# Performance work log

Hardware: AMD Instinct MI355X
Metric: run time of the kernel (lower is better)

## Reference

```python
import jax, jax.numpy as jnp
import numpy as np

B, SL = 16, 512
S = SL - 1            # context length after shift (length=1)
E = 256               # embedding_size / hidden_size
NH = 4                # num_heads
K = 4                 # conv1d_kernel_size
I = 2 * E             # mLSTM inner dim (_inner_embedding_dim = 2*E)
DHM = I // NH         # mLSTM head dim
DHS = E // NH         # sLSTM head dim
NB, BS = I // 4, 4    # qkv_proj_blocksize=4 block-diagonal projections
F = 384               # gated FFN up dim = round_up(1.3*256, 64)
NUM_SKILLS, NUM_Q = 500, 10000
EPS = 1e-5


def _ln(x, w):
    mu = x.mean(-1, keepdims=True)
    var = x.var(-1, keepdims=True)
    return (x - mu) / jnp.sqrt(var + EPS) * w


def _causal_dwconv(x, w, b):
    # x: (B,S,C), depthwise causal conv with kernel (C,K)
    xt = jnp.transpose(x, (0, 2, 1))
    y = jax.lax.conv_general_dilated(
        xt, w[:, None, :], (1,), [(K - 1, 0)],
        dimension_numbers=('NCH', 'OIH', 'NCH'),
        feature_group_count=x.shape[-1])
    return jnp.transpose(y, (0, 2, 1)) + b


def _headwise(x, w):
    # block-diagonal linear: w (NB, BS, BS)
    xb = x.reshape(x.shape[0], x.shape[1], NB, BS)
    return jnp.einsum('bsnd,nod->bsno', xb, w).reshape(x.shape)


def _forward(questions, responses, skills,
             q_embed, qa_embed, q_embed_diff, qa_embed_diff, difficult_param,
             ln0_w, m_up_w, m_up_b, m_conv_w, m_conv_b, m_q_w, m_k_w, m_v_w,
             m_ig_w, m_ig_b, m_fg_w, m_fg_b, m_outnorm_w, m_skip, m_down_w, m_down_b,
             ln1_w, s_conv_w, s_conv_b, s_gate_w, s_rec_w, s_bias, s_gn_w,
             ln2_w, ffn_up_w, ffn_up_b, ffn_down_w, ffn_down_b,
             postnorm_w, out_w1, out_b1, out_w2, out_b2, out_w3, out_b3):
    pid = questions[:, :-1]
    q_data = skills[:, :-1]
    q_shft = skills[:, 1:]
    target = (responses * (responses > -1).astype(responses.dtype))[:, :-1]

    q_e = q_embed[q_data]                              # (B,S,E)
    qa_e = qa_embed[target] + q_e
    pid_e = difficult_param[pid]                       # (B,S,1)
    q_e = q_e + pid_e * q_embed_diff[q_data]
    qa_e = qa_e + pid_e * qa_embed_diff[target]

    # ---- xLSTM stack: block 0 = mLSTM block, block 1 = sLSTM block + gated FFN ----
    x = qa_e  # dropout is identity in eval

    # mLSTM block: x = x + mlstm_layer(LN(x))
    h = _ln(x, ln0_w)
    up = h @ m_up_w.T + m_up_b                         # (B,S,2I)
    x_m, z = jnp.split(up, 2, axis=-1)
    xc = jax.nn.silu(_causal_dwconv(x_m, m_conv_w, m_conv_b))
    q = _headwise(xc, m_q_w)
    k = _headwise(xc, m_k_w)
    v = _headwise(x_m, m_v_w)
    ifin = jnp.concatenate([q, k, v], axis=-1)         # (B,S,3I)
    ig = jnp.einsum('bsf,hf->bhs', ifin, m_ig_w) + m_ig_b[None, :, None]
    fg = jnp.einsum('bsf,hf->bhs', ifin, m_fg_w) + m_fg_b[None, :, None]
    qh = q.reshape(B, S, NH, DHM).transpose(0, 2, 1, 3)
    kh = k.reshape(B, S, NH, DHM).transpose(0, 2, 1, 3)
    vh = v.reshape(B, S, NH, DHM).transpose(0, 2, 1, 3)
    # parallel stabilized mLSTM
    logf = jax.nn.log_sigmoid(fg)                      # (B,NH,S)
    cs = jnp.concatenate([jnp.zeros((B, NH, 1), logf.dtype), jnp.cumsum(logf, -1)], -1)
    dmat = cs[:, :, 1:, None] - cs[:, :, None, 1:]     # (B,NH,S,S): sum of logf over (s,t]
    ltr = jnp.tril(jnp.ones((S, S), bool))
    logD = jnp.where(ltr, dmat, -jnp.inf) + ig[:, :, None, :]
    maxD = jnp.max(logD, -1, keepdims=True)
    D = jnp.exp(logD - maxD)
    qk = jnp.einsum('bhtd,bhsd->bhts', qh, kh) * (DHM ** -0.5)
    C = qk * D
    norm = jnp.maximum(jnp.abs(C.sum(-1, keepdims=True)), jnp.exp(-maxD))
    hh = jnp.einsum('bhts,bhsd->bhtd', C / (norm + 1e-6), vh)
    # multi-head layernorm (per head over DHM), weight on flattened dim
    hn = (hh - hh.mean(-1, keepdims=True)) / jnp.sqrt(hh.var(-1, keepdims=True) + EPS)
    hflat = hn.transpose(0, 2, 1, 3).reshape(B, S, I) * m_outnorm_w
    hout = (hflat + m_skip * xc) * jax.nn.silu(z)
    x = x + (hout @ m_down_w.T + m_down_b)

    # sLSTM block: x = x + slstm_layer(LN(x)); x = x + ffn(LN(x))
    h = _ln(x, ln1_w)
    hc = jax.nn.silu(_causal_dwconv(h, s_conv_w, s_conv_b))
    hh4 = h.reshape(B, S, NH, DHS)
    hc4 = hc.reshape(B, S, NH, DHS)
    gi = jnp.einsum('bsnd,nod->bsno', hc4, s_gate_w[0])   # i,f from conv path
    gf = jnp.einsum('bsnd,nod->bsno', hc4, s_gate_w[1])
    gz = jnp.einsum('bsnd,nod->bsno', hh4, s_gate_w[2])   # z,o from x path
    go = jnp.einsum('bsnd,nod->bsno', hh4, s_gate_w[3])
    wx = jnp.stack([gi, gf, gz, go], axis=2) + s_bias[None, None]  # (B,S,4,NH,DHS)

    def step(carry, wx_t):
        y, c, n, m = carry
        raw = wx_t + jnp.einsum('bnd,gnde->bgne', y, s_rec_w)
        iraw, fraw, zraw, oraw = raw[:, 0], raw[:, 1], raw[:, 2], raw[:, 3]
        logfplusm = m + jax.nn.log_sigmoid(fraw)
        mnew = jnp.maximum(iraw, logfplusm)
        ig_ = jnp.exp(iraw - mnew)
        fg_ = jnp.exp(logfplusm - mnew)
        cnew = fg_ * c + ig_ * jnp.tanh(zraw)
        nnew = fg_ * n + ig_
        ynew = jax.nn.sigmoid(oraw) * cnew / nnew
        return (ynew, cnew, nnew, mnew), ynew

    z0 = jnp.zeros((B, NH, DHS), x.dtype)
    _, ys = jax.lax.scan(step, (z0, z0, z0, z0), jnp.swapaxes(wx, 0, 1))
    y = jnp.swapaxes(ys, 0, 1)                           # (B,S,NH,DHS)
    yn = (y - y.mean(-1, keepdims=True)) / jnp.sqrt(y.var(-1, keepdims=True) + EPS)
    x = x + yn.reshape(B, S, E) * s_gn_w

    # gated FFN (relu)
    h = _ln(x, ln2_w)
    gate, upf = jnp.split(h @ ffn_up_w.T + ffn_up_b, 2, axis=-1)
    x = x + (jax.nn.relu(gate) * upf) @ ffn_down_w.T + ffn_down_b

    d = _ln(x, postnorm_w)                               # post_blocks_norm

    fam = jnp.where((target == 1)[..., None], d, 0.0)
    unfam = jnp.where((target == 0)[..., None], d, 0.0)
    d2 = d - pid_e
    cq = jnp.concatenate([d2, q_e, fam, unfam], axis=-1)  # (B,S,4E)
    o = jax.nn.relu(cq @ out_w1.T + out_b1)
    o = jax.nn.relu(o @ out_w2.T + out_b2)
    probs = jax.nn.sigmoid(o @ out_w3.T + out_b3)
    pred = jnp.take_along_axis(probs, q_shft[..., None], axis=-1)[..., 0]
    return pred                                          # (B,S)


def setup_inputs():
    key = jax.random.key(0)
    ks = iter(jax.random.split(key, 64))
    def rn(shape, s=0.02):
        return jax.random.normal(next(ks), shape, jnp.float32) * s
    return dict(
        questions=jax.random.randint(next(ks), (B, SL), 0, NUM_Q),
        responses=jax.random.randint(next(ks), (B, SL), 0, 2),
        skills=jax.random.randint(next(ks), (B, SL), 0, NUM_SKILLS),
        attention_mask=jnp.ones((B, SL), jnp.int32),
        q_embed=rn((NUM_SKILLS, E), 1.0),
        qa_embed=rn((2, E), 1.0),
        q_embed_diff=rn((NUM_SKILLS + 1, E), 1.0),
        qa_embed_diff=rn((2 * NUM_SKILLS + 1, E), 1.0),
        difficult_param=rn((NUM_Q + 1, 1), 0.1),
        ln0_w=jnp.ones((E,)),
        m_up_w=rn((2 * I, E)), m_up_b=jnp.zeros((2 * I,)),
        m_conv_w=rn((I, K), 0.1), m_conv_b=jnp.zeros((I,)),
        m_q_w=rn((NB, BS, BS), 0.1), m_k_w=rn((NB, BS, BS), 0.1), m_v_w=rn((NB, BS, BS), 0.1),
        m_ig_w=rn((NH, 3 * I)), m_ig_b=jnp.zeros((NH,)),
        m_fg_w=rn((NH, 3 * I)), m_fg_b=jnp.zeros((NH,)),
        m_outnorm_w=jnp.ones((I,)), m_skip=jnp.ones((I,)),
        m_down_w=rn((E, I)), m_down_b=jnp.zeros((E,)),
        ln1_w=jnp.ones((E,)),
        s_conv_w=rn((E, K), 0.1), s_conv_b=jnp.zeros((E,)),
        s_gate_w=rn((4, NH, DHS, DHS), 0.1),
        s_rec_w=rn((4, NH, DHS, DHS), 0.05),
        s_bias=jnp.zeros((4, NH, DHS)),
        s_gn_w=jnp.ones((E,)),
        ln2_w=jnp.ones((E,)),
        ffn_up_w=rn((2 * F, E)), ffn_up_b=jnp.zeros((2 * F,)),
        ffn_down_w=rn((E, F)), ffn_down_b=jnp.zeros((E,)),
        postnorm_w=jnp.ones((E,)),
        out_w1=rn((2 * E, 4 * E)), out_b1=jnp.zeros((2 * E,)),
        out_w2=rn((E, 2 * E)), out_b2=jnp.zeros((E,)),
        out_w3=rn((NUM_SKILLS, E)), out_b3=jnp.zeros((NUM_SKILLS,)),
    )


def reference(questions, responses, skills, attention_mask,
              q_embed, qa_embed, q_embed_diff, qa_embed_diff, difficult_param,
              ln0_w, m_up_w, m_up_b, m_conv_w, m_conv_b, m_q_w, m_k_w, m_v_w,
              m_ig_w, m_ig_b, m_fg_w, m_fg_b, m_outnorm_w, m_skip, m_down_w, m_down_b,
              ln1_w, s_conv_w, s_conv_b, s_gate_w, s_rec_w, s_bias, s_gn_w,
              ln2_w, ffn_up_w, ffn_up_b, ffn_down_w, ffn_down_b,
              postnorm_w, out_w1, out_b1, out_w2, out_b2, out_w3, out_b3):
    return _forward(questions, responses, skills,
                    q_embed, qa_embed, q_embed_diff, qa_embed_diff, difficult_param,
                    ln0_w, m_up_w, m_up_b, m_conv_w, m_conv_b, m_q_w, m_k_w, m_v_w,
                    m_ig_w, m_ig_b, m_fg_w, m_fg_b, m_outnorm_w, m_skip, m_down_w, m_down_b,
                    ln1_w, s_conv_w, s_conv_b, s_gate_w, s_rec_w, s_bias, s_gn_w,
                    ln2_w, ffn_up_w, ffn_up_b, ffn_down_w, ffn_down_b,
                    postnorm_w, out_w1, out_b1, out_w2, out_b2, out_w3, out_b3)
```

## Files before the change

kernel.cpp:

```cpp
#include <hip/hip_runtime.h>
#include <hip/hip_bf16.h>

#define B_    16
#define SL_   512
#define S_    511
#define E_    256
#define NH_   4
#define I_    512
#define DHM_  128
#define DHS_  64
#define F_    384
#define NP_   8192
#define NROW  (B_*S_)
#define EPS_  1e-5f

typedef __hip_bfloat16 bf16;
typedef unsigned short u16;
typedef __bf16 bf16x8v __attribute__((ext_vector_type(8)));
typedef float  f32x4v  __attribute__((ext_vector_type(4)));

__device__ __forceinline__ float rcp_(float x){ return __builtin_amdgcn_rcpf(x); }
__device__ __forceinline__ float sig_(float x){ return rcp_(1.f+__expf(-x)); }
__device__ __forceinline__ float silu_(float x){ return x*sig_(x); }
__device__ __forceinline__ float logsig_(float x){ return fminf(x,0.f) - __logf(1.f + __expf(-fabsf(x))); }
__device__ __forceinline__ float expneg_(float x){ return __expf(fminf(x,0.f)); }
__device__ __forceinline__ float expclamp_(float x){ return __expf(fminf(fmaxf(x,-80.f),80.f)); }
__device__ __forceinline__ float tanh_(float x){ return 1.f - 2.f*rcp_(__expf(2.f*x)+1.f); }

__global__ __launch_bounds__(256) void k_prep(
  const float* __restrict__ m_down_w, bf16* __restrict__ m_down_w16,
  const float* __restrict__ ffn_up_w, bf16* __restrict__ ffn_up_w16,
  const float* __restrict__ ffn_down_w, bf16* __restrict__ ffn_down_w16,
  const float* __restrict__ out_w1, bf16* __restrict__ out_w1_16,
  const float* __restrict__ out_w2, bf16* __restrict__ out_w2_16,
  const float* __restrict__ m_up_w, bf16* __restrict__ m_up_whi, bf16* __restrict__ m_up_wlo,
  const float* __restrict__ s_gate_w, float* __restrict__ gwT,
  const float* __restrict__ s_rec_w, bf16* __restrict__ wfrag)
{
  int i = blockIdx.x*256 + threadIdx.x;
  if (i < 131072){ m_down_w16[i] = __float2bfloat16(m_down_w[i]); return; }
  i -= 131072;
  if (i < 196608){
    int rp=i>>8, c=i&255; int j=rp>>1, p=rp&1;
    ffn_up_w16[i] = __float2bfloat16(ffn_up_w[(size_t)(j + p*F_)*E_ + c]); return;
  }
  i -= 196608;
  if (i < 98304){ ffn_down_w16[i] = __float2bfloat16(ffn_down_w[i]); return; }
  i -= 98304;
  if (i < 524288){ out_w1_16[i] = __float2bfloat16(out_w1[i]); return; }
  i -= 524288;
  if (i < 131072){ out_w2_16[i] = __float2bfloat16(out_w2[i]); return; }
  i -= 131072;
  if (i < 262144){
    float v = m_up_w[i];
    bf16 h = __float2bfloat16(v);
    m_up_whi[i]=h;
    m_up_wlo[i]=__float2bfloat16(v-__bfloat162float(h));
    return;
  }
  i -= 262144;
  if (i < 65536){
    int blk=i>>12, d=(i>>6)&63, e=i&63;
    gwT[(size_t)(blk*64+d)*64+e] = s_gate_w[(size_t)(blk*64+e)*64+d]; return;
  }
  i -= 65536;
  {
    int j=i&7, l=(i>>3)&63, kf=(i>>9)&1, t=(i>>10)&15, n=i>>14;
    int g=t>>2;
    int e=(t&3)*16 + (l&15);
    int d=(l>>4)*16 + kf*8 + j;
    wfrag[i] = __float2bfloat16(s_rec_w[((size_t)((g*4+n)*64 + d))*64 + e]);
  }
}

__global__ __launch_bounds__(256) void k_embed(
  const int* __restrict__ questions, const int* __restrict__ responses, const int* __restrict__ skills,
  const float* __restrict__ q_embed, const float* __restrict__ qa_embed,
  const float* __restrict__ q_embed_diff, const float* __restrict__ qa_embed_diff,
  const float* __restrict__ difficult_param, const float* __restrict__ ln0w,
  float* __restrict__ x, float* __restrict__ qe,
  bf16* __restrict__ h_hi, bf16* __restrict__ h_lo,
  float* __restrict__ pide, int* __restrict__ tgt, int* __restrict__ qsh)
{
  __shared__ float red[256];
  int r = blockIdx.x; int e = threadIdx.x;
  float xa = 0.f;
  if (r < NROW){
    int b = r / S_, s = r % S_;
    int pid  = questions[b*SL_+s];
    int qd   = skills[b*SL_+s];
    int resp = responses[b*SL_+s];
    int t    = (resp > -1) ? resp : 0;
    float pe = difficult_param[pid];
    float q0 = q_embed[qd*E_+e];
    xa = q0 + qa_embed[t*E_+e] + pe*qa_embed_diff[t*E_+e];
    float qn = q0 + pe*q_embed_diff[qd*E_+e];
    x[(size_t)r*E_+e]=xa; qe[(size_t)r*E_+e]=qn;
    if (e==0){ pide[r]=pe; tgt[r]=t; qsh[r]=skills[b*SL_+s+1]; }
  } else {
    x[(size_t)r*E_+e]=0.f; qe[(size_t)r*E_+e]=0.f;
    if (e==0){ pide[r]=0.f; tgt[r]=-7; qsh[r]=0; }
  }
  red[e]=xa; __syncthreads();
  for(int s2=128;s2>0;s2>>=1){ if(e<s2) red[e]+=red[e+s2]; __syncthreads(); }
  float mu = red[0]*(1.f/E_); __syncthreads();
  float d = xa-mu;
  red[e]=d*d; __syncthreads();
  for(int s2=128;s2>0;s2>>=1){ if(e<s2) red[e]+=red[e+s2]; __syncthreads(); }
  float var = red[0]*(1.f/E_);
  float o = d*rsqrtf(var+EPS_)*ln0w[e];
  bf16 hv = __float2bfloat16(o);
  h_hi[(size_t)r*E_+e] = hv;
  h_lo[(size_t)r*E_+e] = __float2bfloat16(o-__bfloat162float(hv));
}

__global__ __launch_bounds__(256) void k_ln(
  const float* __restrict__ in, const float* __restrict__ w, float* __restrict__ out)
{
  __shared__ float red[256];
  int r = blockIdx.x, t = threadIdx.x;
  float v = in[(size_t)r*E_+t];
  red[t]=v; __syncthreads();
  for(int s=128;s>0;s>>=1){ if(t<s) red[t]+=red[t+s]; __syncthreads(); }
  float mu = red[0]*(1.f/E_); __syncthreads();
  float d = v-mu;
  red[t]=d*d; __syncthreads();
  for(int s=128;s>0;s>>=1){ if(t<s) red[t]+=red[t+s]; __syncthreads(); }
  float var = red[0]*(1.f/E_);
  out[(size_t)r*E_+t] = d*rsqrtf(var+EPS_)*w[t];
}

__global__ __launch_bounds__(256) void k_gemm16s(
  const bf16* __restrict__ Ah, const bf16* __restrict__ Al,
  const bf16* __restrict__ Bh, const bf16* __restrict__ Bl,
  const float* __restrict__ bias, float* __restrict__ C, int M, int K)
{
  int tid=threadIdx.x;
  int wave=tid>>6, lane=tid&63;
  int wr=wave>>1, wc=wave&1;
  int row0=blockIdx.y*64 + wr*32;
  int col0=blockIdx.x*64 + wc*32;
  int lrow = lane&15, lq = lane>>4;
  f32x4v acc[2][2] = {};
  size_t aoff = (size_t)(row0+lrow)*K + lq*8;
  size_t boff = (size_t)(col0+lrow)*K + lq*8;
  for(int k0=0;k0<K;k0+=32){
    bf16x8v ah0=*(const bf16x8v*)(Ah+aoff+k0), ah1=*(const bf16x8v*)(Ah+aoff+(size_t)16*K+k0);
    bf16x8v al0=*(const bf16x8v*)(Al+aoff+k0), al1=*(const bf16x8v*)(Al+aoff+(size_t)16*K+k0);
    bf16x8v bh0=*(const bf16x8v*)(Bh+boff+k0), bh1=*(const bf16x8v*)(Bh+boff+(size_t)16*K+k0);
    bf16x8v bl0=*(const bf16x8v*)(Bl+boff+k0), bl1=*(const bf16x8v*)(Bl+boff+(size_t)16*K+k0);
    acc[0][0]=__builtin_amdgcn_mfma_f32_16x16x32_bf16(ah0,bh0,acc[0][0],0,0,0);
    acc[0][1]=__builtin_amdgcn_mfma_f32_16x16x32_bf16(ah0,bh1,acc[0][1],0,0,0);
    acc[1][0]=__builtin_amdgcn_mfma_f32_16x16x32_bf16(ah1,bh0,acc[1][0],0,0,0);
    acc[1][1]=__builtin_amdgcn_mfma_f32_16x16x32_bf16(ah1,bh1,acc[1][1],0,0,0);
    acc[0][0]=__builtin_amdgcn_mfma_f32_16x16x32_bf16(ah0,bl0,acc[0][0],0,0,0);
    acc[0][1]=__builtin_amdgcn_mfma_f32_16x16x32_bf16(ah0,bl1,acc[0][1],0,0,0);
    acc[1][0]=__builtin_amdgcn_mfma_f32_16x16x32_bf16(ah1,bl0,acc[1][0],0,0,0);
    acc[1][1]=__builtin_amdgcn_mfma_f32_16x16x32_bf16(ah1,bl1,acc[1][1],0,0,0);
    acc[0][0]=__builtin_amdgcn_mfma_f32_16x16x32_bf16(al0,bh0,acc[0][0],0,0,0);
    acc[0][1]=__builtin_amdgcn_mfma_f32_16x16x32_bf16(al0,bh1,acc[0][1],0,0,0);
    acc[1][0]=__builtin_amdgcn_mfma_f32_16x16x32_bf16(al1,bh0,acc[1][0],0,0,0);
    acc[1][1]=__builtin_amdgcn_mfma_f32_16x16x32_bf16(al1,bh1,acc[1][1],0,0,0);
  }
  #pragma unroll
  for(int mi=0;mi<2;mi++){
    #pragma unroll
    for(int ni=0;ni<2;ni++){
      #pragma unroll
      for(int r=0;r<4;r++){
        int row=row0+mi*16+lq*4+r;
        int col=col0+ni*16+lrow;
        C[(size_t)row*M+col]=acc[mi][ni][r] + bias[col];
      }
    }
  }
}

__global__ __launch_bounds__(256) void k_gemm16(
  const bf16* __restrict__ A, const bf16* __restrict__ Bw,
  const float* __restrict__ bias, const float* __restrict__ resid,
  float* __restrict__ C, bf16* __restrict__ C16,
  int M, int K, int relu)
{
  int tid=threadIdx.x;
  int wave=tid>>6, lane=tid&63;
  int wr=wave>>1, wc=wave&1;
  int row0=blockIdx.y*64 + wr*32;
  int col0=blockIdx.x*64 + wc*32;
  int lrow = lane&15, lq = lane>>4;
  f32x4v acc[2][2] = {};
  const bf16* Abase = A  + (size_t)(row0+lrow)*K + lq*8;
  const bf16* Bbase = Bw + (size_t)(col0+lrow)*K + lq*8;
  for(int k0=0;k0<K;k0+=32){
    bf16x8v a0 = *(const bf16x8v*)(Abase + k0);
    bf16x8v a1 = *(const bf16x8v*)(Abase + (size_t)16*K + k0);
    bf16x8v b0 = *(const bf16x8v*)(Bbase + k0);
    bf16x8v b1 = *(const bf16x8v*)(Bbase + (size_t)16*K + k0);
    acc[0][0]=__builtin_amdgcn_mfma_f32_16x16x32_bf16(a0,b0,acc[0][0],0,0,0);
    acc[0][1]=__builtin_amdgcn_mfma_f32_16x16x32_bf16(a0,b1,acc[0][1],0,0,0);
    acc[1][0]=__builtin_amdgcn_mfma_f32_16x16x32_bf16(a1,b0,acc[1][0],0,0,0);
    acc[1][1]=__builtin_amdgcn_mfma_f32_16x16x32_bf16(a1,b1,acc[1][1],0,0,0);
  }
  #pragma unroll
  for(int mi=0;mi<2;mi++){
    #pragma unroll
    for(int ni=0;ni<2;ni++){
      #pragma unroll
      for(int r=0;r<4;r++){
        int row=row0+mi*16+lq*4+r;
        int col=col0+ni*16+lrow;
        float v=acc[mi][ni][r] + (bias? bias[col]:0.f);
        if(relu) v=fmaxf(v,0.f);
        if(resid) v += resid[(size_t)row*M+col];
        if(C)   C[(size_t)row*M+col]=v;
        if(C16) C16[(size_t)row*M+col]=__float2bfloat16(v);
      }
    }
  }
}

__global__ __launch_bounds__(256) void k_gemm16f(
  const bf16* __restrict__ A, const bf16* __restrict__ Bw,
  const float* __restrict__ bias, bf16* __restrict__ out, int K)
{
  int tid=threadIdx.x;
  int wave=tid>>6, lane=tid&63;
  int wr=wave>>1, wc=wave&1;
  int row0=blockIdx.y*64 + wr*32;
  int col0=blockIdx.x*64 + wc*32;
  int lrow = lane&15, lq = lane>>4;
  f32x4v acc[2][2] = {};
  const bf16* Abase = A  + (size_t)(row0+lrow)*K + lq*8;
  const bf16* Bbase = Bw + (size_t)(col0+lrow)*K + lq*8;
  for(int k0=0;k0<K;k0+=32){
    bf16x8v a0 = *(const bf16x8v*)(Abase + k0);
    bf16x8v a1 = *(const bf16x8v*)(Abase + (size_t)16*K + k0);
    bf16x8v b0 = *(const bf16x8v*)(Bbase + k0);
    bf16x8v b1 = *(const bf16x8v*)(Bbase + (size_t)16*K + k0);
    acc[0][0]=__builtin_amdgcn_mfma_f32_16x16x32_bf16(a0,b0,acc[0][0],0,0,0);
    acc[0][1]=__builtin_amdgcn_mfma_f32_16x16x32_bf16(a0,b1,acc[0][1],0,0,0);
    acc[1][0]=__builtin_amdgcn_mfma_f32_16x16x32_bf16(a1,b0,acc[1][0],0,0,0);
    acc[1][1]=__builtin_amdgcn_mfma_f32_16x16x32_bf16(a1,b1,acc[1][1],0,0,0);
  }
  #pragma unroll
  for(int mi=0;mi<2;mi++){
    #pragma unroll
    for(int ni=0;ni<2;ni++){
      #pragma unroll
      for(int r=0;r<4;r++){
        int row=row0+mi*16+lq*4+r;
        int col=col0+ni*16+lrow;
        float v=acc[mi][ni][r] + bias[(col>>1) + (col&1)*F_];
        float o = __shfl_xor(v, 1, 64);
        if(!(lrow&1)){
          out[(size_t)row*F_ + (col>>1)] = __float2bfloat16(fmaxf(v,0.f)*o);
        }
      }
    }
  }
}

__global__ __launch_bounds__(256) void k_conv_silu(
  const float* __restrict__ in, int ild, const float* __restrict__ w, const float* __restrict__ bws,
  float* __restrict__ out, int old_, int C)
{
  int i = blockIdx.x*256 + threadIdx.x;
  int r = i / C, c = i % C;
  if (r >= NP_) return;
  float acc = 0.f;
  if (r < NROW) {
    int b=r/S_, s=r%S_;
    acc = bws[c];
    #pragma unroll
    for(int j=0;j<4;j++){
      int ss=s-3+j;
      if(ss>=0) acc += w[c*4+j] * in[(size_t)(b*S_+ss)*ild + c];
    }
    acc = silu_(acc);
  }
  out[(size_t)r*old_ + c] = acc;
}

__global__ __launch_bounds__(256) void k_mega(
  const float* __restrict__ A,
  const float* __restrict__ cw, const float* __restrict__ cb,
  const float* __restrict__ wq, const float* __restrict__ wk, const float* __restrict__ wv,
  const float* __restrict__ wig, const float* __restrict__ big,
  const float* __restrict__ wfg, const float* __restrict__ bfg,
  float* __restrict__ xcout,
  bf16* __restrict__ qhi, bf16* __restrict__ qlo,
  bf16* __restrict__ khi, bf16* __restrict__ klo,
  bf16* __restrict__ vhi, bf16* __restrict__ vlo,
  float* __restrict__ igb, float* __restrict__ fgb)
{
  __shared__ float xcs[512];
  __shared__ float xms[512];
  __shared__ float qs[512], ks[512], vs[512];
  int r = blockIdx.x;
  int tid = threadIdx.x;
  if (r >= NROW){
    bf16 z = __float2bfloat16(0.f);
    size_t o = (size_t)r*512 + tid*2;
    qhi[o]=z; qhi[o+1]=z; qlo[o]=z; qlo[o+1]=z;
    khi[o]=z; khi[o+1]=z; klo[o]=z; klo[o+1]=z;
    vhi[o]=z; vhi[o+1]=z; vlo[o]=z; vlo[o+1]=z;
    return;
  }
  int b=r/S_, s=r%S_;
  const float* arow = A + (size_t)r*1024;
  for (int c=tid; c<512; c+=256){
    float acc = cb[c];
    #pragma unroll
    for(int j=0;j<4;j++){
      int ss=s-3+j;
      if(ss>=0) acc += cw[c*4+j]*A[((size_t)(b*S_+ss))*1024 + c];
    }
    acc = silu_(acc);
    xcs[c]=acc;
    xcout[(size_t)r*512+c]=acc;
    xms[c]=arow[c];
  }
  __syncthreads();
  for (int c=tid; c<512; c+=256){
    int n=c>>2, o=c&3;
    float aq=0.f, ak=0.f, av=0.f;
    #pragma unroll
    for(int d=0;d<4;d++){
      aq += xcs[n*4+d]*wq[(n*4+o)*4+d];
      ak += xcs[n*4+d]*wk[(n*4+o)*4+d];
      av += xms[n*4+d]*wv[(n*4+o)*4+d];
    }
    qs[c]=aq; ks[c]=ak; vs[c]=av;
    size_t oi=(size_t)r*512+c;
    bf16 qh=__float2bfloat16(aq); qhi[oi]=qh; qlo[oi]=__float2bfloat16(aq-__bfloat162float(qh));
    bf16 kh=__float2bfloat16(ak); khi[oi]=kh; klo[oi]=__float2bfloat16(ak-__bfloat162float(kh));
    bf16 vh=__float2bfloat16(av); vhi[oi]=vh; vlo[oi]=__float2bfloat16(av-__bfloat162float(vh));
  }
  __syncthreads();
  int h = tid>>6, lane = tid&63;
  float ai=0.f, af=0.f;
  for(int f=lane; f<1536; f+=64){
    float val = (f<512)? qs[f] : (f<1024)? ks[f-512] : vs[f-1024];
    ai += val*wig[h*1536+f];
    af += val*wfg[h*1536+f];
  }
  for(int m=32;m;m>>=1){ ai+=__shfl_xor(ai,m,64); af+=__shfl_xor(af,m,64); }
  if(lane==0){
    igb[(b*4+h)*512+s]=ai+big[h];
    fgb[(b*4+h)*512+s]=af+bfg[h];
  }
}

__global__ __launch_bounds__(256) void k_decay(
  const float* __restrict__ igb, const float* __restrict__ fgb,
  float* __restrict__ cs1, float* __restrict__ g, float* __restrict__ M)
{
  int bh = blockIdx.x; int tid = threadIdx.x;
  __shared__ float buf[512];
  __shared__ float buf2[512];
  for (int s=tid; s<512; s+=256)
    buf[s] = (s<S_) ? logsig_(fgb[bh*512+s]) : 0.f;
  __syncthreads();
  for (int off=1; off<512; off<<=1){
    int s0=tid, s1=tid+256;
    float v0 = buf[s0] + ((s0>=off)? buf[s0-off] : 0.f);
    float v1 = buf[s1] + ((s1>=off)? buf[s1-off] : 0.f);
    __syncthreads();
    buf[s0]=v0; buf[s1]=v1;
    __syncthreads();
  }
  for (int s=tid; s<512; s+=256){
    float c = buf[s];
    if (s<S_){
      cs1[bh*512+s]=c;
      float gv = igb[bh*512+s]-c;
      g[bh*512+s]=gv;
      buf2[s]=gv;
    } else buf2[s] = -3.4e38f;
  }
  __syncthreads();
  for (int off=1; off<512; off<<=1){
    int s0=tid, s1=tid+256;
    float v0 = fmaxf(buf2[s0], (s0>=off)? buf2[s0-off] : -3.4e38f);
    float v1 = fmaxf(buf2[s1], (s1>=off)? buf2[s1-off] : -3.4e38f);
    __syncthreads();
    buf2[s0]=v0; buf2[s1]=v1;
    __syncthreads();
  }
  for (int s=tid; s<S_; s+=256) M[bh*512+s] = buf2[s];
}

#define TQ 32
#define TS 32
__global__ __launch_bounds__(256) void k_attn(
  const bf16* __restrict__ qhi, const bf16* __restrict__ qlo,
  const bf16* __restrict__ khi, const bf16* __restrict__ klo,
  const bf16* __restrict__ vhi, const bf16* __restrict__ vlo,
  const float* __restrict__ cs1, const float* __restrict__ g, const float* __restrict__ M,
  const float* __restrict__ onw, const float* __restrict__ skip,
  const float* __restrict__ xc, const float* __restrict__ zA,
  bf16* __restrict__ out16)
{
  __shared__ __align__(16) u16 vThi[128][40];
  __shared__ __align__(16) u16 vTlo[128][40];
  __shared__ __align__(16) u16 phi[32][40];
  __shared__ __align__(16) u16 plo[32][40];
  __shared__ float MtS[32], cssS[32], normS[32], muS[32], rsS[32];
  __shared__ float lsumW[2][32], sumA[2][32], sumB[2][32];

  int tq = blockIdx.x, bh = blockIdx.y;
  int b = bh>>2, h = bh&3;
  int tid = threadIdx.x;
  int wv = tid>>6;
  int tw = wv&1, sw = wv>>1;
  int l = tid&63;
  int lr = l&15, lg = l>>4;
  int t0 = tq*TQ;
  const float sc = 0.08838834764831843f;

  if (tid < 32){
    int t = t0 + tid; int tc = (t<S_)? t : (S_-1);
    MtS[tid]  = M[bh*512 + tc];
    cssS[tid] = cs1[bh*512 + tc];
  }

  bf16x8v qh[4], ql[4];
  {
    size_t qoff = ((size_t)(b*S_ + t0 + tw*16 + lr))*512 + h*128 + lg*8;
    #pragma unroll
    for(int k0=0;k0<4;k0++){
      qh[k0] = *(const bf16x8v*)(qhi + qoff + k0*32);
      ql[k0] = *(const bf16x8v*)(qlo + qoff + k0*32);
    }
  }

  f32x4v accpv[4] = {};
  float lsum[4] = {0.f,0.f,0.f,0.f};

  int t1 = min(t0+TQ, S_);
  int sp = tid>>4, dl = tid&15;

  __syncthreads();

  for (int s0=0; s0<t1; s0+=TS){
    bf16x8v kh[4], kl2[4];
    {
      size_t koff = ((size_t)(b*S_ + s0 + sw*16 + lr))*512 + h*128 + lg*8;
      #pragma unroll
      for(int k0=0;k0<4;k0++){
        kh[k0]  = *(const bf16x8v*)(khi + koff + k0*32);
        kl2[k0] = *(const bf16x8v*)(klo + koff + k0*32);
      }
    }
    u16 vha[8], vhb[8], vla[8], vlb[8];
    {
      const u16* ha = (const u16*)vhi + ((size_t)(b*S_ + s0 + 2*sp))*512 + h*128 + dl;
      const u16* la = (const u16*)vlo + ((size_t)(b*S_ + s0 + 2*sp))*512 + h*128 + dl;
      #pragma unroll
      for(int j=0;j<8;j++){
        vha[j]=ha[16*j]; vhb[j]=ha[512+16*j];
        vla[j]=la[16*j]; vlb[j]=la[512+16*j];
      }
    }
    float g_s = g[bh*512 + s0 + sw*16 + lr];

    f32x4v cqk = {0.f,0.f,0.f,0.f};
    #pragma unroll
    for(int k0=0;k0<4;k0++){
      cqk = __builtin_amdgcn_mfma_f32_16x16x32_bf16(qh[k0], kh[k0],  cqk, 0,0,0);
      cqk = __builtin_amdgcn_mfma_f32_16x16x32_bf16(qh[k0], kl2[k0], cqk, 0,0,0);
      cqk = __builtin_amdgcn_mfma_f32_16x16x32_bf16(ql[k0], kh[k0],  cqk, 0,0,0);
    }

    int s_g = s0 + sw*16 + lr;
    u16 pw_h[4], pw_l[4];
    #pragma unroll
    for(int r=0;r<4;r++){
      int tl = tw*16 + lg*4 + r;
      int t_row = t0 + tl;
      float wvv = ((s_g <= t_row) && (t_row < S_)) ? cqk[r]*sc*expneg_(g_s - MtS[tl]) : 0.f;
      lsum[r] += wvv;
      bf16 hh = __float2bfloat16(wvv);
      float hf = __bfloat162float(hh);
      bf16 ll = __float2bfloat16(wvv - hf);
      __builtin_memcpy(&pw_h[r], &hh, 2);
      __builtin_memcpy(&pw_l[r], &ll, 2);
    }

    __syncthreads();

    #pragma unroll
    for(int r=0;r<4;r++){
      int tl = tw*16 + lg*4 + r;
      phi[tl][sw*16 + lr] = pw_h[r];
      plo[tl][sw*16 + lr] = pw_l[r];
    }
    {
      unsigned* vh32 = (unsigned*)&vThi[0][0];
      unsigned* vl32 = (unsigned*)&vTlo[0][0];
      #pragma unroll
      for(int j=0;j<8;j++){
        int d = dl + 16*j;
        vh32[d*20 + sp] = (unsigned)vha[j] | ((unsigned)vhb[j]<<16);
        vl32[d*20 + sp] = (unsigned)vla[j] | ((unsigned)vlb[j]<<16);
      }
    }

    __syncthreads();

    bf16x8v pah = *(const bf16x8v*)((const void*)(&phi[tw*16 + lr][0] + lg*8));
    bf16x8v pal = *(const bf16x8v*)((const void*)(&plo[tw*16 + lr][0] + lg*8));
    #pragma unroll
    for(int fd=0; fd<4; fd++){
      bf16x8v vbh = *(const bf16x8v*)((const void*)(&vThi[sw*64 + fd*16 + lr][0] + lg*8));
      bf16x8v vbl = *(const bf16x8v*)((const void*)(&vTlo[sw*64 + fd*16 + lr][0] + lg*8));
      accpv[fd] = __builtin_amdgcn_mfma_f32_16x16x32_bf16(pah, vbh, accpv[fd], 0,0,0);
      accpv[fd] = __builtin_amdgcn_mfma_f32_16x16x32_bf16(pah, vbl, accpv[fd], 0,0,0);
      accpv[fd] = __builtin_amdgcn_mfma_f32_16x16x32_bf16(pal, vbh, accpv[fd], 0,0,0);
    }
  }

  #pragma unroll
  for(int r=0;r<4;r++){
    #pragma unroll
    for(int m=1;m<16;m<<=1) lsum[r] += __shfl_xor(lsum[r], m, 16);
  }
  if (lr==0){
    #pragma unroll
    for(int r=0;r<4;r++) lsumW[sw][tw*16 + lg*4 + r] = lsum[r];
  }
  __syncthreads();
  if (tid < 32){
    float ls = lsumW[0][tid] + lsumW[1][tid];
    float maxD = cssS[tid] + MtS[tid];
    float nrm = fmaxf(fabsf(ls), expclamp_(-maxD));
    normS[tid] = rcp_(nrm + 1e-6f);
  }
  __syncthreads();

  float o_[4][4];
  float srow[4]={0.f,0.f,0.f,0.f}, sq[4]={0.f,0.f,0.f,0.f};
  #pragma unroll
  for(int r=0;r<4;r++){
    float scl = normS[tw*16 + lg*4 + r];
    #pragma unroll
    for(int fd=0;fd<4;fd++){
      float o = accpv[fd][r]*scl;
      o_[fd][r] = o;
      srow[r] += o; sq[r] += o*o;
    }
  }
  #pragma unroll
  for(int r=0;r<4;r++){
    #pragma unroll
    for(int m=1;m<16;m<<=1){ srow[r]+=__shfl_xor(srow[r],m,16); sq[r]+=__shfl_xor(sq[r],m,16); }
  }
  if (lr==0){
    #pragma unroll
    for(int r=0;r<4;r++){ sumA[sw][tw*16+lg*4+r]=srow[r]; sumB[sw][tw*16+lg*4+r]=sq[r]; }
  }
  __syncthreads();
  if (tid < 32){
    float mu = (sumA[0][tid]+sumA[1][tid])*(1.f/128.f);
    float ex2= (sumB[0][tid]+sumB[1][tid])*(1.f/128.f);
    muS[tid]=mu;
    rsS[tid]=rsqrtf(fmaxf(ex2 - mu*mu, 0.f)+EPS_);
  }
  __syncthreads();

  #pragma unroll
  for(int fd=0; fd<4; fd++){
    int d = sw*64 + fd*16 + lr;
    float ow = onw[h*128 + d];
    float sk = skip[h*128 + d];
    #pragma unroll
    for(int r=0;r<4;r++){
      int tl = tw*16 + lg*4 + r;
      int t = t0 + tl;
      if (t < S_){
        size_t row = (size_t)(b*S_+t);
        float hf = (o_[fd][r]-muS[tl])*rsS[tl]*ow;
        float xcv = xc[row*512 + h*128 + d];
        float zv  = zA[row*1024 + 512 + h*128 + d];
        out16[row*512 + h*128 + d] = __float2bfloat16((hf + sk*xcv)*silu_(zv));
      }
    }
  }
}

#define WXR 64
__global__ __launch_bounds__(256,2) void k_wx(
  const float* __restrict__ h, const float* __restrict__ hc,
  const float* __restrict__ gwT, const float* __restrict__ gb,
  float* __restrict__ wx)
{
  int rt = blockIdx.x, g = blockIdx.y;
  int tid = threadIdx.x;
  int n = tid>>6, e = tid&63;
  const float* src = (g<2)? hc : h;
  __shared__ __align__(16) float hs[WXR][260];
  float W[64];
  #pragma unroll
  for(int d=0;d<64;d++) W[d] = gwT[(size_t)(((g*4+n)*64+d))*64 + e];
  float bias = gb[(g*4+n)*64+e];
  int row0 = rt*WXR;
  for(int idx=tid; idx<WXR*64; idx+=256){
    int rr = idx>>6, cc4 = (idx&63)*4;
    *(float4*)&hs[rr][cc4] = *(const float4*)(src + (size_t)(row0+rr)*256 + cc4);
  }
  __syncthreads();
  #pragma unroll 4
  for(int rr=0; rr<WXR; ++rr){
    int r = row0+rr;
    if (r>=NROW) break;
    const float* hrow = &hs[rr][n*64];
    float a0=0,a1=0,a2=0,a3=0;
    #pragma unroll
    for(int d=0;d<64;d+=4){
      float4 hv = *(const float4*)&hrow[d];
      a0+=hv.x*W[d]; a1+=hv.y*W[d+1]; a2+=hv.z*W[d+2]; a3+=hv.w*W[d+3];
    }
    int b=r/S_, s=r%S_;
    wx[(((size_t)(b*4+n)*512 + s)*256) + e*4 + g] = bias + ((a0+a1)+(a2+a3));
  }
}

__global__ __launch_bounds__(256,1) void k_scan(
  const float* __restrict__ wx, const bf16* __restrict__ wf, float* __restrict__ y_out)
{
  int bn = blockIdx.x; int b = bn>>2, n = bn&3;
  int tid = threadIdx.x;
  int w = tid>>6;
  int l = tid&63;
  int q = l>>4;
  int el = l&15;
  int e  = w*16 + el;

  __shared__ __align__(16) unsigned short ybuf[2][64];

  if (tid < 128) ((unsigned short*)ybuf)[tid] = 0;
  __syncthreads();

  bf16x8v Wf2[4][2];
  #pragma unroll
  for(int g=0; g<4; ++g){
    #pragma unroll
    for(int kf=0; kf<2; ++kf){
      Wf2[g][kf] = *(const bf16x8v*)(wf + ((size_t)((n*16 + (4*g+w))*2 + kf)*64 + l)*8);
    }
  }

  const float* wxBase = wx + ((size_t)bn*512)*256 + e*4;
  float* yst = y_out + (size_t)(b*S_)*256 + n*64 + e;

  float4 p0,p1,p2,p3;
  p0 = *(const float4*)(wxBase + (size_t)0*256);
  p1 = *(const float4*)(wxBase + (size_t)1*256);
  p2 = *(const float4*)(wxBase + (size_t)2*256);
  p3 = *(const float4*)(wxBase + (size_t)3*256);

  f32x4v z4 = {0.f,0.f,0.f,0.f};
  float c=0.f, nn=0.f, pm=1.f;

  for (int s=0; s<S_; ++s){
    int p = s&1;
    bf16x8v a0 = *(const bf16x8v*)&ybuf[p][16*q];
    bf16x8v a1 = *(const bf16x8v*)&ybuf[p][16*q+8];

    f32x4v acc0,acc1,acc2,acc3, accb0,accb1,accb2,accb3;
    acc0  = __builtin_amdgcn_mfma_f32_16x16x32_bf16(a0, Wf2[0][0], z4, 0,0,0);
    acc1  = __builtin_amdgcn_mfma_f32_16x16x32_bf16(a0, Wf2[1][0], z4, 0,0,0);
    acc2  = __builtin_amdgcn_mfma_f32_16x16x32_bf16(a0, Wf2[2][0], z4, 0,0,0);
    acc3  = __builtin_amdgcn_mfma_f32_16x16x32_bf16(a0, Wf2[3][0], z4, 0,0,0);
    accb0 = __builtin_amdgcn_mfma_f32_16x16x32_bf16(a1, Wf2[0][1], z4, 0,0,0);
    accb1 = __builtin_amdgcn_mfma_f32_16x16x32_bf16(a1, Wf2[1][1], z4, 0,0,0);
    accb2 = __builtin_amdgcn_mfma_f32_16x16x32_bf16(a1, Wf2[2][1], z4, 0,0,0);
    accb3 = __builtin_amdgcn_mfma_f32_16x16x32_bf16(a1, Wf2[3][1], z4, 0,0,0);

    float4 wg = p0; p0=p1; p1=p2; p2=p3;
    { int sp = s+4; if (sp>510) sp=510;
      p3 = *(const float4*)(wxBase + (size_t)sp*256); }

    float iraw=acc0[0]+accb0[0]+wg.x, fraw=acc1[0]+accb1[0]+wg.y;
    float zraw=acc2[0]+accb2[0]+wg.z, oraw=acc3[0]+accb3[0]+wg.w;

    float pe  = __expf(fminf(iraw, 80.f));
    float ef  = __expf(-fraw);
    float e2z = __expf(2.f*zraw);
    float eo  = __expf(-oraw);
    float sf  = rcp_(1.f+ef);
    float ps  = pm*sf;
    float pn  = fmaxf(fmaxf(pe, ps), 1e-30f);
    float rpn = rcp_(pn);
    float fg  = ps*rpn;
    float ig  = pe*rpn;
    float th  = 1.f - 2.f*rcp_(e2z+1.f);
    c  = fg*c + ig*th;
    nn = fmaxf(fg*nn + ig, 1e-30f);
    float y = rcp_(1.f+eo) * c * rcp_(nn);
    pm = pn;

    bf16 hb = __float2bfloat16(y);
    unsigned short hbits; __builtin_memcpy(&hbits,&hb,2);
    if (l < 16){
      ybuf[p^1][e] = hbits;
      yst[(size_t)s*256] = y;
    }
    asm volatile("s_waitcnt lgkmcnt(0)" ::: "memory");
    __builtin_amdgcn_s_barrier();
    asm volatile("" ::: "memory");
    __builtin_amdgcn_sched_barrier(0);
  }
}

__global__ __launch_bounds__(256) void k_ynadd_ln2(
  const float* __restrict__ y, const float* __restrict__ gn,
  float* __restrict__ x, const float* __restrict__ ln2w, bf16* __restrict__ h16)
{
  __shared__ float red[256];
  int r=blockIdx.x, t=threadIdx.x;
  float xv = x[(size_t)r*256+t];
  if (r < NROW){
    float v=y[(size_t)r*256+t];
    float s=v;
    for(int m=32;m;m>>=1) s+=__shfl_xor(s,m,64);
    float mu=s*(1.f/64.f);
    float d=v-mu;
    float q=d*d;
    for(int m=32;m;m>>=1) q+=__shfl_xor(q,m,64);
    float var=q*(1.f/64.f);
    xv += d*rsqrtf(var+EPS_)*gn[t];
    x[(size_t)r*256+t]=xv;
  }
  red[t]=xv; __syncthreads();
  for(int s=128;s>0;s>>=1){ if(t<s) red[t]+=red[t+s]; __syncthreads(); }
  float mu2=red[0]*(1.f/E_); __syncthreads();
  float dd=xv-mu2;
  red[t]=dd*dd; __syncthreads();
  for(int s=128;s>0;s>>=1){ if(t<s) red[t]+=red[t+s]; __syncthreads(); }
  float var2=red[0]*(1.f/E_);
  h16[(size_t)r*256+t]=__float2bfloat16(dd*rsqrtf(var2+EPS_)*ln2w[t]);
}

__global__ __launch_bounds__(256) void k_cq_ln(
  const float* __restrict__ x, const float* __restrict__ pw,
  const float* __restrict__ qe, const float* __restrict__ pide, const int* __restrict__ tgt,
  bf16* __restrict__ cq)
{
  __shared__ float red[256];
  int r=blockIdx.x, t=threadIdx.x;
  float v = x[(size_t)r*256+t];
  red[t]=v; __syncthreads();
  for(int s=128;s>0;s>>=1){ if(t<s) red[t]+=red[t+s]; __syncthreads(); }
  float mu=red[0]*(1.f/E_); __syncthreads();
  float d=v-mu;
  red[t]=d*d; __syncthreads();
  for(int s=128;s>0;s>>=1){ if(t<s) red[t]+=red[t+s]; __syncthreads(); }
  float var=red[0]*(1.f/E_);
  float dv = d*rsqrtf(var+EPS_)*pw[t];
  float pe=pide[r]; int tg=tgt[r];
  size_t base=(size_t)r*1024;
  cq[base+t]=__float2bfloat16(dv-pe);
  cq[base+256+t]=__float2bfloat16(qe[(size_t)r*256+t]);
  cq[base+512+t]=__float2bfloat16((tg==1)? dv:0.f);
  cq[base+768+t]=__float2bfloat16((tg==0)? dv:0.f);
}

__global__ __launch_bounds__(256) void k_final(
  const float* __restrict__ o2, const float* __restrict__ w3, const float* __restrict__ b3,
  const int* __restrict__ qsh, float* __restrict__ out)
{
  __shared__ float red[256];
  int r=blockIdx.x, t=threadIdx.x;
  int qi=qsh[r];
  float p=o2[(size_t)r*256+t]*w3[(size_t)qi*256+t];
  red[t]=p; __syncthreads();
  for(int s=128;s>0;s>>=1){ if(t<s) red[t]+=red[t+s]; __syncthreads(); }
  if(t==0) out[r]=sig_(red[0]+b3[qi]);
}

extern "C" void kernel_launch(void* const* d_in, const int* in_sizes, int n_in,
                              void* d_out, int out_size, void* d_ws, size_t ws_size,
                              hipStream_t stream) {
  const int* questions = (const int*)d_in[0];
  const int* responses = (const int*)d_in[1];
  const int* skills    = (const int*)d_in[2];
  const float* q_embed       = (const float*)d_in[4];
  const float* qa_embed      = (const float*)d_in[5];
  const float* q_embed_diff  = (const float*)d_in[6];
  const float* qa_embed_diff = (const float*)d_in[7];
  const float* difficult_param=(const float*)d_in[8];
  const float* ln0_w   = (const float*)d_in[9];
  const float* m_up_w  = (const float*)d_in[10];
  const float* m_up_b  = (const float*)d_in[11];
  const float* m_conv_w= (const float*)d_in[12];
  const float* m_conv_b= (const float*)d_in[13];
  const float* m_q_w   = (const float*)d_in[14];
  const float* m_k_w   = (const float*)d_in[15];
  const float* m_v_w   = (const float*)d_in[16];
  const float* m_ig_w  = (const float*)d_in[17];
  const float* m_ig_b  = (const float*)d_in[18];
  const float* m_fg_w  = (const float*)d_in[19];
  const float* m_fg_b  = (const float*)d_in[20];
  const float* m_outnorm_w=(const float*)d_in[21];
  const float* m_skip  = (const float*)d_in[22];
  const float* m_down_w= (const float*)d_in[23];
  const float* m_down_b= (const float*)d_in[24];
  const float* ln1_w   = (const float*)d_in[25];
  const float* s_conv_w= (const float*)d_in[26];
  const float* s_conv_b= (const float*)d_in[27];
  const float* s_gate_w= (const float*)d_in[28];
  const float* s_rec_w = (const float*)d_in[29];
  const float* s_bias  = (const float*)d_in[30];
  const float* s_gn_w  = (const float*)d_in[31];
  const float* ln2_w   = (const float*)d_in[32];
  const float* ffn_up_w= (const float*)d_in[33];
  const float* ffn_up_b= (const float*)d_in[34];
  const float* ffn_down_w=(const float*)d_in[35];
  const float* ffn_down_b=(const float*)d_in[36];
  const float* postnorm_w=(const float*)d_in[37];
  const float* out_w1  = (const float*)d_in[38];
  const float* out_b1  = (const float*)d_in[39];
  const float* out_w2  = (const float*)d_in[40];
  const float* out_b2  = (const float*)d_in[41];
  const float* out_w3  = (const float*)d_in[42];
  const float* out_b3  = (const float*)d_in[43];

  float* ws = (float*)d_ws;
  const size_t R = (size_t)NP_*256;
  float* x    = ws;
  float* qe   = ws + R;
  float* h    = ws + 2*R;
  float* t256 = ws + 3*R;
  float* A    = ws + 4*R;
  float* Bb   = ws + 8*R;
  float* Cb   = ws + 10*R;
  float* Db   = ws + 12*R;
  float* Eb   = ws + 14*R;
  float* pide = ws + 16*R;
  int*   tgt  = (int*)(ws + 16*R + NP_);
  int*   qsh  = (int*)(ws + 16*R + 2*NP_);
  float* igb  = ws + 16*R + 3*NP_;
  float* fgb  = igb + 64*512;
  float* cs1  = fgb + 64*512;
  float* gdec = cs1 + 64*512;
  float* Mrun = gdec + 64*512;
  bf16* wpool = (bf16*)(Mrun + 64*512);
  bf16* m_down_w16  = wpool;
  bf16* ffn_up_w16  = m_down_w16 + 256*512;
  bf16* ffn_down_w16= ffn_up_w16 + 768*256;
  bf16* out_w1_16   = ffn_down_w16 + 256*384;
  bf16* out_w2_16   = out_w1_16 + 512*1024;
  bf16* h16         = out_w2_16 + 256*512;
  bf16* m_up_whi    = h16 + (size_t)NP_*256;
  bf16* m_up_wlo    = m_up_whi + 1024*256;
  float* gwT        = (float*)(m_up_wlo + 1024*256);
  bf16* wfrag       = (bf16*)(gwT + 16*64*64);
  bf16* q_hi = (bf16*)Cb;  bf16* q_lo = q_hi + (size_t)NP_*512;
  bf16* k_hi = (bf16*)Db;  bf16* k_lo = k_hi + (size_t)NP_*512;
  bf16* v_hi = (bf16*)Eb;  bf16* v_lo = v_hi + (size_t)NP_*512;
  bf16* hout16 = (bf16*)h;
  bf16* ffg16  = (bf16*)Db;
  bf16* cq16   = (bf16*)Eb;
  bf16* b16    = (bf16*)Cb;
  bf16* h_hi   = (bf16*)t256;
  bf16* h_lo   = h_hi + (size_t)NP_*256;

  k_prep<<<5760,256,0,stream>>>(
      m_down_w, m_down_w16, ffn_up_w, ffn_up_w16, ffn_down_w, ffn_down_w16,
      out_w1, out_w1_16, out_w2, out_w2_16, m_up_w, m_up_whi, m_up_wlo,
      s_gate_w, gwT, s_rec_w, wfrag);

  k_embed<<<NP_,256,0,stream>>>(questions,responses,skills,q_embed,qa_embed,
      q_embed_diff,qa_embed_diff,difficult_param, ln0_w, x,qe, h_hi,h_lo, pide,tgt,qsh);
  k_gemm16s<<<dim3(1024/64,NP_/64),256,0,stream>>>(h_hi,h_lo, m_up_whi,m_up_wlo, m_up_b, A, 1024,256);
  k_mega<<<NP_,256,0,stream>>>(A, m_conv_w,m_conv_b, m_q_w,m_k_w,m_v_w,
      m_ig_w,m_ig_b,m_fg_w,m_fg_b, Bb, q_hi,q_lo, k_hi,k_lo, v_hi,v_lo, igb,fgb);
  k_decay<<<64,256,0,stream>>>(igb,fgb, cs1,gdec,Mrun);
  hipMemsetAsync(hout16 + (size_t)NROW*512, 0, (size_t)(NP_-NROW)*512*sizeof(bf16), stream);
  k_attn<<<dim3((S_+TQ-1)/TQ, B_*NH_),256,0,stream>>>(q_hi,q_lo, k_hi,k_lo, v_hi,v_lo,
      cs1,gdec,Mrun, m_outnorm_w, m_skip, Bb, A, hout16);
  k_gemm16<<<dim3(256/64,NP_/64),256,0,stream>>>(hout16, m_down_w16, m_down_b, x, x, (bf16*)nullptr, 256,512,0);
  k_ln<<<NP_,256,0,stream>>>(x, ln1_w, h);
  k_conv_silu<<<(NP_*256)/256,256,0,stream>>>(h,256, s_conv_w,s_conv_b, Bb,256,256);
  k_wx<<<dim3(128,4),256,0,stream>>>(h, Bb, gwT, s_bias, A);
  k_scan<<<64,256,0,stream>>>(A, wfrag, Cb);
  k_ynadd_ln2<<<NP_,256,0,stream>>>(Cb, s_gn_w, x, ln2_w, h16);
  k_gemm16f<<<dim3(768/64,NP_/64),256,0,stream>>>(h16, ffn_up_w16, ffn_up_b, ffg16, 256);
  k_gemm16<<<dim3(256/64,NP_/64),256,0,stream>>>(ffg16, ffn_down_w16, ffn_down_b, x, x, (bf16*)nullptr, 256,384,0);
  k_cq_ln<<<NP_,256,0,stream>>>(x, postnorm_w, qe, pide, tgt, cq16);
  k_gemm16<<<dim3(512/64,NP_/64),256,0,stream>>>(cq16, out_w1_16, out_b1, (const float*)nullptr, (float*)nullptr, b16, 512,1024,1);
  k_gemm16<<<dim3(256/64,NP_/64),256,0,stream>>>(b16, out_w2_16, out_b2, (const float*)nullptr, t256, (bf16*)nullptr, 256,512,1);
  k_final<<<NROW,256,0,stream>>>(t256, out_w3, out_b3, qsh, (float*)d_out);
}
```

Baseline: 800.4 us.

## Fuse LN1, causal conv+SiLU and gate projection into one kernel; use wave-shuffle reductions

Replaces the separate layernorm, depthwise causal conv+SiLU and gate-projection kernels with a single kernel. It recomputes LN1 for 16 rows plus a 3-row halo in shared memory, applies the conv from there, and feeds both tensors to the gate matmul, so the intermediate h and conv buffers are never written to or read from global memory. Separately, the tree reductions in the other layernorm and final kernels become 64-lane shuffle reductions with a 4-wave combine, which cuts the number of barriers. The cost is that each block recomputes LN and conv for every gate group (4x redundancy), the block tile shrinks from 64 to 16 rows, and the 64 gate weights are reloaded per block, which raises weight-load overhead.

After: 813.4 us. About the same (+1.6%).

```diff
diff --git a/kernel.cpp b/kernel.cpp
--- a/kernel.cpp
+++ b/kernel.cpp
@@ -82,7 +82,7 @@
   bf16* __restrict__ h_hi, bf16* __restrict__ h_lo,
   float* __restrict__ pide, int* __restrict__ tgt, int* __restrict__ qsh)
 {
-  __shared__ float red[256];
+  __shared__ float pA[4], pB[4];
   int r = blockIdx.x; int e = threadIdx.x;
   float xa = 0.f;
   if (r < NROW){
@@ -101,33 +101,21 @@
     x[(size_t)r*E_+e]=0.f; qe[(size_t)r*E_+e]=0.f;
     if (e==0){ pide[r]=0.f; tgt[r]=-7; qsh[r]=0; }
   }
-  red[e]=xa; __syncthreads();
-  for(int s2=128;s2>0;s2>>=1){ if(e<s2) red[e]+=red[e+s2]; __syncthreads(); }
-  float mu = red[0]*(1.f/E_); __syncthreads();
+  float s_ = xa;
+  for(int m=32;m;m>>=1) s_ += __shfl_xor(s_,m,64);
+  if((e&63)==0) pA[e>>6]=s_;
+  __syncthreads();
+  float mu = (pA[0]+pA[1]+pA[2]+pA[3])*(1.f/E_);
   float d = xa-mu;
-  red[e]=d*d; __syncthreads();
-  for(int s2=128;s2>0;s2>>=1){ if(e<s2) red[e]+=red[e+s2]; __syncthreads(); }
-  float var = red[0]*(1.f/E_);
+  float q_ = d*d;
+  for(int m=32;m;m>>=1) q_ += __shfl_xor(q_,m,64);
+  if((e&63)==0) pB[e>>6]=q_;
+  __syncthreads();
+  float var = (pB[0]+pB[1]+pB[2]+pB[3])*(1.f/E_);
   float o = d*rsqrtf(var+EPS_)*ln0w[e];
   bf16 hv = __float2bfloat16(o);
   h_hi[(size_t)r*E_+e] = hv;
   h_lo[(size_t)r*E_+e] = __float2bfloat16(o-__bfloat162float(hv));
-}
-
-__global__ __launch_bounds__(256) void k_ln(
-  const float* __restrict__ in, const float* __restrict__ w, float* __restrict__ out)
-{
-  __shared__ float red[256];
-  int r = blockIdx.x, t = threadIdx.x;
-  float v = in[(size_t)r*E_+t];
-  red[t]=v; __syncthreads();
-  for(int s=128;s>0;s>>=1){ if(t<s) red[t]+=red[t+s]; __syncthreads(); }
-  float mu = red[0]*(1.f/E_); __syncthreads();
-  float d = v-mu;
-  red[t]=d*d; __syncthreads();
-  for(int s=128;s>0;s>>=1){ if(t<s) red[t]+=red[t+s]; __syncthreads(); }
-  float var = red[0]*(1.f/E_);
-  out[(size_t)r*E_+t] = d*rsqrtf(var+EPS_)*w[t];
 }
 
 __global__ __launch_bounds__(256) void k_gemm16s(
@@ -260,27 +248,6 @@
   }
 }
 
-__global__ __launch_bounds__(256) void k_conv_silu(
-  const float* __restrict__ in, int ild, const float* __restrict__ w, const float* __restrict__ bws,
-  float* __restrict__ out, int old_, int C)
-{
-  int i = blockIdx.x*256 + threadIdx.x;
-  int r = i / C, c = i % C;
-  if (r >= NP_) return;
-  float acc = 0.f;
-  if (r < NROW) {
-    int b=r/S_, s=r%S_;
-    acc = bws[c];
-    #pragma unroll
-    for(int j=0;j<4;j++){
-      int ss=s-3+j;
-      if(ss>=0) acc += w[c*4+j] * in[(size_t)(b*S_+ss)*ild + c];
-    }
-    acc = silu_(acc);
-  }
-  out[(size_t)r*old_ + c] = acc;
-}
-
 __global__ __launch_bounds__(256) void k_mega(
   const float* __restrict__ A,
   const float* __restrict__ cw, const float* __restrict__ cb,
@@ -588,32 +555,68 @@
   }
 }
 
-#define WXR 64
-__global__ __launch_bounds__(256,2) void k_wx(
-  const float* __restrict__ h, const float* __restrict__ hc,
+#define SWR 16
+__global__ __launch_bounds__(256) void k_swx(
+  const float* __restrict__ x, const float* __restrict__ ln1w,
+  const float* __restrict__ cw, const float* __restrict__ cb,
   const float* __restrict__ gwT, const float* __restrict__ gb,
   float* __restrict__ wx)
 {
+  __shared__ __align__(16) float hs[SWR+3][260];
+  __shared__ __align__(16) float hcs[SWR][260];
   int rt = blockIdx.x, g = blockIdx.y;
   int tid = threadIdx.x;
+  int wv = tid>>6, lane = tid&63;
+  int r0 = rt*SWR;
+  if (r0 >= NROW) return;
+  for (int i=wv; i<SWR+3; i+=4){
+    int r = r0 - 3 + i;
+    if (r < 0 || r >= NROW){
+      for(int c=lane;c<256;c+=64) hs[i][c]=0.f;
+      continue;
+    }
+    const float* xr = x + (size_t)r*256;
+    float v0=xr[lane], v1=xr[lane+64], v2=xr[lane+128], v3=xr[lane+192];
+    float s_ = v0+v1+v2+v3;
+    for(int m=32;m;m>>=1) s_ += __shfl_xor(s_,m,64);
+    float mu = s_*(1.f/256.f);
+    float d0=v0-mu,d1=v1-mu,d2=v2-mu,d3=v3-mu;
+    float q_ = d0*d0+d1*d1+d2*d2+d3*d3;
+    for(int m=32;m;m>>=1) q_ += __shfl_xor(q_,m,64);
+    float rs = rsqrtf(q_*(1.f/256.f)+EPS_);
+    hs[i][lane]     = d0*rs*ln1w[lane];
+    hs[i][lane+64]  = d1*rs*ln1w[lane+64];
+    hs[i][lane+128] = d2*rs*ln1w[lane+128];
+    hs[i][lane+192] = d3*rs*ln1w[lane+192];
+  }
+  __syncthreads();
+  {
+    int c = tid;
+    if (c < 256){
+      for (int rr=0; rr<SWR; ++rr){
+        int r = r0+rr;
+        if (r>=NROW) break;
+        int s = r % S_;
+        float acc = cb[c];
+        #pragma unroll
+        for(int j=0;j<4;j++){
+          int ss = s-3+j;
+          if (ss>=0) acc += cw[c*4+j]*hs[rr+j][c];
+        }
+        hcs[rr][c] = silu_(acc);
+      }
+    }
+  }
+  __syncthreads();
   int n = tid>>6, e = tid&63;
-  const float* src = (g<2)? hc : h;
-  __shared__ __align__(16) float hs[WXR][260];
   float W[64];
   #pragma unroll
   for(int d=0;d<64;d++) W[d] = gwT[(size_t)(((g*4+n)*64+d))*64 + e];
   float bias = gb[(g*4+n)*64+e];
-  int row0 = rt*WXR;
-  for(int idx=tid; idx<WXR*64; idx+=256){
-    int rr = idx>>6, cc4 = (idx&63)*4;
-    *(float4*)&hs[rr][cc4] = *(const float4*)(src + (size_t)(row0+rr)*256 + cc4);
-  }
-  __syncthreads();
-  #pragma unroll 4
-  for(int rr=0; rr<WXR; ++rr){
-    int r = row0+rr;
+  for (int rr=0; rr<SWR; ++rr){
+    int r = r0+rr;
     if (r>=NROW) break;
-    const float* hrow = &hs[rr][n*64];
+    const float* hrow = (g<2)? &hcs[rr][n*64] : &hs[rr+3][n*64];
     float a0=0,a1=0,a2=0,a3=0;
     #pragma unroll
     for(int d=0;d<64;d+=4){
@@ -717,7 +720,7 @@
   const float* __restrict__ y, const float* __restrict__ gn,
   float* __restrict__ x, const float* __restrict__ ln2w, bf16* __restrict__ h16)
 {
-  __shared__ float red[256];
+  __shared__ float pA[4], pB[4];
   int r=blockIdx.x, t=threadIdx.x;
   float xv = x[(size_t)r*256+t];
   if (r < NROW){
@@ -732,13 +735,17 @@
     xv += d*rsqrtf(var+EPS_)*gn[t];
     x[(size_t)r*256+t]=xv;
   }
-  red[t]=xv; __syncthreads();
-  for(int s=128;s>0;s>>=1){ if(t<s) red[t]+=red[t+s]; __syncthreads(); }
-  float mu2=red[0]*(1.f/E_); __syncthreads();
+  float s2 = xv;
+  for(int m=32;m;m>>=1) s2 += __shfl_xor(s2,m,64);
+  if((t&63)==0) pA[t>>6]=s2;
+  __syncthreads();
+  float mu2=(pA[0]+pA[1]+pA[2]+pA[3])*(1.f/E_);
   float dd=xv-mu2;
-  red[t]=dd*dd; __syncthreads();
-  for(int s=128;s>0;s>>=1){ if(t<s) red[t]+=red[t+s]; __syncthreads(); }
-  float var2=red[0]*(1.f/E_);
+  float q2=dd*dd;
+  for(int m=32;m;m>>=1) q2 += __shfl_xor(q2,m,64);
+  if((t&63)==0) pB[t>>6]=q2;
+  __syncthreads();
+  float var2=(pB[0]+pB[1]+pB[2]+pB[3])*(1.f/E_);
   h16[(size_t)r*256+t]=__float2bfloat16(dd*rsqrtf(var2+EPS_)*ln2w[t]);
 }
 
@@ -747,16 +754,20 @@
   const float* __restrict__ qe, const float* __restrict__ pide, const int* __restrict__ tgt,
   bf16* __restrict__ cq)
 {
-  __shared__ float red[256];
+  __shared__ float pA[4], pB[4];
   int r=blockIdx.x, t=threadIdx.x;
   float v = x[(size_t)r*256+t];
-  red[t]=v; __syncthreads();
-  for(int s=128;s>0;s>>=1){ if(t<s) red[t]+=red[t+s]; __syncthreads(); }
-  float mu=red[0]*(1.f/E_); __syncthreads();
+  float s_=v;
+  for(int m=32;m;m>>=1) s_ += __shfl_xor(s_,m,64);
+  if((t&63)==0) pA[t>>6]=s_;
+  __syncthreads();
+  float mu=(pA[0]+pA[1]+pA[2]+pA[3])*(1.f/E_);
   float d=v-mu;
-  red[t]=d*d; __syncthreads();
-  for(int s=128;s>0;s>>=1){ if(t<s) red[t]+=red[t+s]; __syncthreads(); }
-  float var=red[0]*(1.f/E_);
+  float q_=d*d;
+  for(int m=32;m;m>>=1) q_ += __shfl_xor(q_,m,64);
+  if((t&63)==0) pB[t>>6]=q_;
+  __syncthreads();
+  float var=(pB[0]+pB[1]+pB[2]+pB[3])*(1.f/E_);
   float dv = d*rsqrtf(var+EPS_)*pw[t];
   float pe=pide[r]; int tg=tgt[r];
   size_t base=(size_t)r*1024;
@@ -770,13 +781,14 @@
   const float* __restrict__ o2, const float* __restrict__ w3, const float* __restrict__ b3,
   const int* __restrict__ qsh, float* __restrict__ out)
 {
-  __shared__ float red[256];
+  __shared__ float pA[4];
   int r=blockIdx.x, t=threadIdx.x;
   int qi=qsh[r];
   float p=o2[(size_t)r*256+t]*w3[(size_t)qi*256+t];
-  red[t]=p; __syncthreads();
-  for(int s=128;s>0;s>>=1){ if(t<s) red[t]+=red[t+s]; __syncthreads(); }
-  if(t==0) out[r]=sig_(red[0]+b3[qi]);
+  for(int m=32;m;m>>=1) p += __shfl_xor(p,m,64);
+  if((t&63)==0) pA[t>>6]=p;
+  __syncthreads();
+  if(t==0) out[r]=sig_(pA[0]+pA[1]+pA[2]+pA[3]+b3[qi]);
 }
 
 extern "C" void kernel_launch(void* const* d_in, const int* in_sizes, int n_in,
@@ -881,9 +893,7 @@
   k_attn<<<dim3((S_+TQ-1)/TQ, B_*NH_),256,0,stream>>>(q_hi,q_lo, k_hi,k_lo, v_hi,v_lo,
       cs1,gdec,Mrun, m_outnorm_w, m_skip, Bb, A, hout16);
   k_gemm16<<<dim3(256/64,NP_/64),256,0,stream>>>(hout16, m_down_w16, m_down_b, x, x, (bf16*)nullptr, 256,512,0);
-  k_ln<<<NP_,256,0,stream>>>(x, ln1_w, h);
-  k_conv_silu<<<(NP_*256)/256,256,0,stream>>>(h,256, s_conv_w,s_conv_b, Bb,256,256);
-  k_wx<<<dim3(128,4),256,0,stream>>>(h, Bb, gwT, s_bias, A);
+  k_swx<<<dim3((NROW+SWR-1)/SWR,4),256,0,stream>>>(x, ln1_w, s_conv_w, s_conv_b, gwT, s_bias, A);
   k_scan<<<64,256,0,stream>>>(A, wfrag, Cb);
   k_ynadd_ln2<<<NP_,256,0,stream>>>(Cb, s_gn_w, x, ln2_w, h16);
   k_gemm16f<<<dim3(768/64,NP_/64),256,0,stream>>>(h16, ffn_up_w16, ffn_up_b, ffg16, 256);
```
